# Optimization experiments

Measured on AMD Instinct MI355X. Metric: run time of the kernel, lower is better.

Reference implementation:

```python
import jax, jax.numpy as jnp
import numpy as np

SPARSITY_W = 0.01
SMOOTH_W = 0.1
K = 10  # min(10, N-1) with N >> 10


def setup_inputs() -> dict:
    key = jax.random.key(0)
    k1, k2, k3 = jax.random.split(key, 3)
    N = 16384
    positions = jax.random.normal(k1, (N, 3), dtype=jnp.float32)
    opacities = jax.random.uniform(k2, (N,), dtype=jnp.float32)
    scales = jax.random.uniform(k3, (N, 3), dtype=jnp.float32)
    return {"positions": positions, "opacities": opacities, "scales": scales}


def _pairwise_dist(x):
    # Euclidean cdist(x, x): [N, N]
    sq = jnp.sum(x * x, axis=-1)
    d2 = sq[:, None] + sq[None, :] - 2.0 * (x @ x.T)
    return jnp.sqrt(jnp.maximum(d2, 0.0))


def reference(positions, opacities, scales):
    # sparsity: mean |opacity|
    sparsity_loss = jnp.mean(jnp.abs(opacities))

    # smoothness: kNN (k=10, excluding self) gather + mean |opacity diff|
    dist = _pairwise_dist(positions)                       # [N, N]
    _, idx = jax.lax.top_k(-dist, K + 1)                   # smallest K+1 dists
    nbr_idx = idx[:, 1:]                                   # drop self: [N, K]
    nbr_op = opacities[nbr_idx]                            # [N, K]
    smoothness_loss = jnp.mean(jnp.abs(opacities[:, None] - nbr_op))

    # scale reg: mean |scale - 1|
    scale_loss = jnp.mean(jnp.abs(scales - 1.0))

    # opacity reg: mean (opacity - 0.5)^2
    opacity_loss = jnp.mean((opacities - 0.5) ** 2)

    return (SPARSITY_W * sparsity_loss + SMOOTH_W * smoothness_loss
            + scale_loss + opacity_loss)
```

## Files before the change

kernel.cpp:

```cpp
#include <hip/hip_runtime.h>
#include <stdint.h>

#define NPTS   16384
#define TOPK   10
#define NBX    32
#define NBK    (32 * 32 * 32)
#define XMIN   (-5.0f)
#define INVBW  (3.2f)
#define SENT_STEP 0x4000u
#define NSLOT  256


__device__ __forceinline__ unsigned umin_(unsigned a, unsigned b) { return a < b ? a : b; }
__device__ __forceinline__ unsigned umax_(unsigned a, unsigned b) { return a > b ? a : b; }

__device__ __forceinline__ void chain_insert(unsigned a[TOPK], unsigned key) {
#pragma unroll
    for (int k = TOPK - 1; k > 0; --k) a[k] = umin_(umax_(a[k - 1], key), a[k]);
    a[0] = umin_(a[0], key);
}

__device__ __forceinline__ void ce_(unsigned &x, unsigned &y) {
    unsigned lo = umin_(x, y); y = umax_(x, y); x = lo;
}

__device__ __forceinline__ void bitonic10(unsigned a[TOPK]) {
    ce_(a[0], a[8]); ce_(a[1], a[9]);
    ce_(a[0], a[4]); ce_(a[1], a[5]); ce_(a[2], a[6]); ce_(a[3], a[7]);
    ce_(a[0], a[2]); ce_(a[1], a[3]); ce_(a[4], a[6]); ce_(a[5], a[7]);
    ce_(a[0], a[1]); ce_(a[2], a[3]); ce_(a[4], a[5]); ce_(a[6], a[7]); ce_(a[8], a[9]);
}

__device__ __forceinline__ void merge_shfl(unsigned a[TOPK], int w) {
    unsigned b[TOPK];
#pragma unroll
    for (int k = 0; k < TOPK; ++k) b[k] = (unsigned)__shfl_xor((int)a[k], w, 64);
#pragma unroll
    for (int k = 0; k < TOPK; ++k) a[k] = umin_(a[k], b[TOPK - 1 - k]);
    bitonic10(a);
}

__device__ __forceinline__ void scan2(
    unsigned a[TOPK], const float4* __restrict__ sorted,
    unsigned p0, unsigned p1, unsigned s, float mx, float my, float mz)
{
    float4 c0 = sorted[p0];
    float4 c1 = sorted[p1];
    float dx0 = c0.x - mx, dy0 = c0.y - my, dz0 = c0.z - mz;
    float dx1 = c1.x - mx, dy1 = c1.y - my, dz1 = c1.z - mz;
    float d20 = fmaf(dx0, dx0, fmaf(dy0, dy0, dz0 * dz0));
    float d21 = fmaf(dx1, dx1, fmaf(dy1, dy1, dz1 * dz1));
    unsigned k0 = (__float_as_uint(d20) & 0xFFFFC000u) | p0;
    unsigned k1 = (__float_as_uint(d21) & 0xFFFFC000u) | p1;
    if (p0 == s) k0 = 0xFFFFFFFFu;
    if (p1 == s) k1 = 0xFFFFFFFFu;
    unsigned kmin = umin_(k0, k1), kmax = umax_(k0, k1);
    if (kmin < a[TOPK - 1]) {
        chain_insert(a, kmin);
        if (kmax < a[TOPK - 1]) chain_insert(a, kmax);
    }
}

__device__ __forceinline__ void scan1(
    unsigned a[TOPK], const float4* __restrict__ sorted,
    unsigned p, unsigned s, float mx, float my, float mz)
{
    float4 c = sorted[p];
    float dx = c.x - mx, dy = c.y - my, dz = c.z - mz;
    float d2 = fmaf(dx, dx, fmaf(dy, dy, dz * dz));
    unsigned key = (__float_as_uint(d2) & 0xFFFFC000u) | p;
    if (p == s) key = 0xFFFFFFFFu;
    if (key < a[TOPK - 1]) chain_insert(a, key);
}

__device__ __forceinline__ int cellf(float v) {
    int b = (int)((v - XMIN) * INVBW);
    return min(max(b, 0), NBX - 1);
}

__global__ __launch_bounds__(256) void setup_kernel(
    const float* __restrict__ pos, const float* __restrict__ opac,
    const float* __restrict__ scales, float* __restrict__ parts,
    unsigned* __restrict__ hist)
{
    int i = blockIdx.x * 256 + threadIdx.x;
    float o = opac[i];
    float d = o - 0.5f;
    float s_sp = fabsf(o);
    float s_op = d * d;
    float s_sc = fabsf(scales[3 * i] - 1.0f) + fabsf(scales[3 * i + 1] - 1.0f)
               + fabsf(scales[3 * i + 2] - 1.0f);
    int bx = cellf(pos[3 * i]);
    int by = cellf(pos[3 * i + 1]);
    int bz = cellf(pos[3 * i + 2]);
    atomicAdd(&hist[(bx << 10) | (by << 5) | bz], 1u);
#pragma unroll
    for (int off = 32; off > 0; off >>= 1) {
        s_sp += __shfl_down(s_sp, off, 64);
        s_sc += __shfl_down(s_sc, off, 64);
        s_op += __shfl_down(s_op, off, 64);
    }
    if ((threadIdx.x & 63) == 0) {
        const int row = (blockIdx.x * 4 + (threadIdx.x >> 6)) & (NSLOT - 1);
        atomicAdd(&parts[row * 32 + 0], s_sp);
        atomicAdd(&parts[row * 32 + 1], s_sc);
        atomicAdd(&parts[row * 32 + 2], s_op);
    }
}

__global__ __launch_bounds__(1024) void prefix_scan(
    unsigned* __restrict__ hist, unsigned* __restrict__ base)
{
    __shared__ unsigned wsum[16];
    const int t = threadIdx.x;
    const int lane = t & 63, wid = t >> 6;
    unsigned loc[32];
    uint4* h4 = (uint4*)(hist + t * 32);
#pragma unroll
    for (int j = 0; j < 8; ++j) {
        uint4 h = h4[j];
        loc[4 * j + 0] = h.x; loc[4 * j + 1] = h.y;
        loc[4 * j + 2] = h.z; loc[4 * j + 3] = h.w;
    }
    unsigned run = 0;
#pragma unroll
    for (int j = 0; j < 32; ++j) { unsigned v = loc[j]; loc[j] = run; run += v; }
    unsigned inc = run;
#pragma unroll
    for (int off = 1; off < 64; off <<= 1) {
        unsigned v = (unsigned)__shfl_up((int)inc, off, 64);
        if (lane >= off) inc += v;
    }
    if (lane == 63) wsum[wid] = inc;
    __syncthreads();
    if (wid == 0) {
        unsigned w = (lane < 16) ? wsum[lane] : 0u;
#pragma unroll
        for (int off = 1; off < 16; off <<= 1) {
            unsigned v = (unsigned)__shfl_up((int)w, off, 64);
            if (lane >= off) w += v;
        }
        if (lane < 16) wsum[lane] = w;
    }
    __syncthreads();
    const unsigned wbase = (wid > 0) ? wsum[wid - 1] : 0u;
    const unsigned tbase = wbase + inc - run;
    uint4* b4 = (uint4*)(base + t * 32);
#pragma unroll
    for (int j = 0; j < 8; ++j) {
        b4[j] = make_uint4(loc[4 * j] + tbase, loc[4 * j + 1] + tbase,
                           loc[4 * j + 2] + tbase, loc[4 * j + 3] + tbase);
        h4[j] = make_uint4(0u, 0u, 0u, 0u);
    }
    if (t == 1023) base[NBK] = NPTS;
}

__global__ __launch_bounds__(256) void scatter_sorted(
    const float* __restrict__ pos, const float* __restrict__ opac,
    const unsigned* __restrict__ base, unsigned* __restrict__ cnt,
    float4* __restrict__ sorted)
{
    int i = blockIdx.x * 256 + threadIdx.x;
    float x = pos[3 * i], y = pos[3 * i + 1], z = pos[3 * i + 2];
    int b = (cellf(x) << 10) | (cellf(y) << 5) | cellf(z);
    unsigned p = base[b] + atomicAdd(&cnt[b], 1u);
    sorted[p] = make_float4(x, y, z, opac[i]);
}

__global__ __launch_bounds__(256) void knn_all(
    const float4* __restrict__ sorted, const unsigned* __restrict__ base,
    float* __restrict__ parts)
{
    const int lane = threadIdx.x & 63;
    const int s    = (blockIdx.x * 256 + threadIdx.x) >> 6;

    const float4 me = sorted[s];

    unsigned a[TOPK];
#pragma unroll
    for (int k = 0; k < TOPK; ++k) a[k] = 0xFFFFFFFFu;
    {
        const int dir = lane >> 5;
        const int start = 1 + (lane & 31) * 4;
#pragma unroll
        for (int t = 0; t < 4; ++t) {
            int p = dir ? (s - start - t) : (s + start + t);
            int pc = min(max(p, 0), NPTS - 1);
            float4 c = sorted[pc];
            float dx = c.x - me.x, dy = c.y - me.y, dz = c.z - me.z;
            float d2 = fmaf(dx, dx, fmaf(dy, dy, dz * dz));
            unsigned key = (__float_as_uint(d2) & 0xFFFFC000u) | (unsigned)pc;
            if (p < 0 || p >= NPTS) key = 0xFFFFFFFFu;
            chain_insert(a, key);
        }
    }
    merge_shfl(a, 1);  merge_shfl(a, 2);  merge_shfl(a, 4);
    merge_shfl(a, 8);  merge_shfl(a, 16); merge_shfl(a, 32);
    const unsigned sentinel = (a[TOPK - 1] & 0xFFFFC000u) + SENT_STEP;
    const float R = sqrtf(__uint_as_float(sentinel)) + 1e-6f;

    const int bxlo = cellf(me.x - R), bxhi = cellf(me.x + R);
    const int bylo = cellf(me.y - R), byhi = cellf(me.y + R);
    const int bzlo = cellf(me.z - R), bzhi = cellf(me.z + R);
    const int nyw   = byhi - bylo + 1;
    const int npair = (bxhi - bxlo + 1) * nyw;

#pragma unroll
    for (int k = 0; k < TOPK; ++k) a[k] = sentinel;

    const int grp = lane >> 3;
    const int gl  = lane & 7;

    for (int cbase = 0; cbase < npair; cbase += 64) {
        const int cnum = min(64, npair - cbase);
        unsigned mylo = 0, myhi = 0;
        const int pi = cbase + lane;
        if (pi < npair) {
            const int qx = pi / nyw;
            const int cb = ((bxlo + qx) << 10) | ((bylo + pi - qx * nyw) << 5);
            mylo = base[cb + bzlo];
            myhi = base[cb + bzhi + 1];
        }
        for (int j = grp; j < cnum; j += 8) {
            const unsigned lo = (unsigned)__shfl((int)mylo, j, 64);
            const unsigned hi = (unsigned)__shfl((int)myhi, j, 64);
            unsigned p = lo + gl;
            for (; p + 8 < hi; p += 16)
                scan2(a, sorted, p, p + 8, (unsigned)s, me.x, me.y, me.z);
            if (p < hi)
                scan1(a, sorted, p, (unsigned)s, me.x, me.y, me.z);
        }
    }

    merge_shfl(a, 1);  merge_shfl(a, 2);  merge_shfl(a, 4);
    merge_shfl(a, 8);  merge_shfl(a, 16); merge_shfl(a, 32);

    float v = 0.0f;
    if (lane < TOPK) {
        int j = (int)(a[lane] & 0x3FFFu);
        v = fabsf(me.w - sorted[j].w);
    }
    v += __shfl_down(v, 8, 64);
    v += __shfl_down(v, 4, 64);
    v += __shfl_down(v, 2, 64);
    v += __shfl_down(v, 1, 64);
    if (lane == 0)
        atomicAdd(&parts[(s & (NSLOT - 1)) * 32 + 3], v);
}

__global__ void combine(const float* __restrict__ parts, float* __restrict__ out)
{
    const int lane = threadIdx.x;
    float sp = 0.0f, sc = 0.0f, op = 0.0f, sm = 0.0f;
#pragma unroll
    for (int r = 0; r < NSLOT / 64; ++r) {
        float4 p = *(const float4*)(parts + (r * 64 + lane) * 32);
        sp += p.x; sc += p.y; op += p.z; sm += p.w;
    }
#pragma unroll
    for (int off = 32; off > 0; off >>= 1) {
        sp += __shfl_down(sp, off, 64);
        sc += __shfl_down(sc, off, 64);
        op += __shfl_down(op, off, 64);
        sm += __shfl_down(sm, off, 64);
    }
    if (lane == 0) {
        const float n = (float)NPTS;
        out[0] = 0.01f * (sp / n) + 0.1f * (sm / (n * 10.0f))
               + sc / (3.0f * n) + op / n;
    }
}

extern "C" void kernel_launch(void* const* d_in, const int* in_sizes, int n_in,
                              void* d_out, int out_size, void* d_ws, size_t ws_size,
                              hipStream_t stream)
{
    const float* pos    = (const float*)d_in[0];
    const float* opac   = (const float*)d_in[1];
    const float* scales = (const float*)d_in[2];
    float* out = (float*)d_out;

    char* ws = (char*)d_ws;
    float*    parts  = (float*)(ws + 128);
    unsigned* histcnt= (unsigned*)(ws + 33024);
    unsigned* base   = (unsigned*)(ws + 164096);
    float4*   sorted = (float4*)(ws + 295296);

    hipMemsetAsync(ws, 0, 164096, stream);

    setup_kernel  <<<NPTS / 256, 256, 0, stream>>>(pos, opac, scales, parts, histcnt);
    prefix_scan   <<<1, 1024, 0, stream>>>(histcnt, base);
    scatter_sorted<<<NPTS / 256, 256, 0, stream>>>(pos, opac, base, histcnt, sorted);
    knn_all       <<<NPTS / 4, 256, 0, stream>>>(sorted, base, parts);
    combine       <<<1, 64, 0, stream>>>(parts, out);
}
```

Before: 112.8 us.

## Fuse histogram, scan and scatter into one cooperative kernel; sort initial kNN keys

Merges the setup, single-block prefix scan and scatter kernels into one cooperative kernel with grid-wide syncs. The atomic rank from the histogram pass is reused for the scatter, so the second atomic pass is gone, and the scan is spread over 64 blocks. This removes two launch gaps and the serial single-block scan, at the cost of three grid.sync barriers. It also replaces four chain inserts in the kNN seeding with a 4-element sorting network before the shuffle merges.

```diff
diff --git a/kernel.cpp b/kernel.cpp
--- a/kernel.cpp
+++ b/kernel.cpp
@@ -1,5 +1,8 @@
 #include <hip/hip_runtime.h>
+#include <hip/hip_cooperative_groups.h>
 #include <stdint.h>
+
+namespace cg = cooperative_groups;
 
 #define NPTS   16384
 #define TOPK   10
@@ -9,6 +12,7 @@
 #define INVBW  (3.2f)
 #define SENT_STEP 0x4000u
 #define NSLOT  256
+#define PRE_BLOCKS 64
 
 
 __device__ __forceinline__ unsigned umin_(unsigned a, unsigned b) { return a < b ? a : b; }
@@ -78,93 +82,77 @@
     return min(max(b, 0), NBX - 1);
 }
 
-__global__ __launch_bounds__(256) void setup_kernel(
+__global__ __launch_bounds__(256) void preprocess(
     const float* __restrict__ pos, const float* __restrict__ opac,
     const float* __restrict__ scales, float* __restrict__ parts,
-    unsigned* __restrict__ hist)
-{
-    int i = blockIdx.x * 256 + threadIdx.x;
-    float o = opac[i];
+    unsigned* __restrict__ hist, unsigned* __restrict__ blocksum,
+    unsigned* __restrict__ base, float4* __restrict__ sorted)
+{
+    cg::grid_group grid = cg::this_grid();
+    const int tid  = blockIdx.x * 256 + threadIdx.x;
+    const int lane = threadIdx.x & 63;
+    const int wv   = threadIdx.x >> 6;
+
+    const float x = pos[3 * tid], y = pos[3 * tid + 1], z = pos[3 * tid + 2];
+    const float o = opac[tid];
     float d = o - 0.5f;
     float s_sp = fabsf(o);
     float s_op = d * d;
-    float s_sc = fabsf(scales[3 * i] - 1.0f) + fabsf(scales[3 * i + 1] - 1.0f)
-               + fabsf(scales[3 * i + 2] - 1.0f);
-    int bx = cellf(pos[3 * i]);
-    int by = cellf(pos[3 * i + 1]);
-    int bz = cellf(pos[3 * i + 2]);
-    atomicAdd(&hist[(bx << 10) | (by << 5) | bz], 1u);
+    float s_sc = fabsf(scales[3 * tid] - 1.0f) + fabsf(scales[3 * tid + 1] - 1.0f)
+               + fabsf(scales[3 * tid + 2] - 1.0f);
+    const int b = (cellf(x) << 10) | (cellf(y) << 5) | cellf(z);
+    const unsigned rank = atomicAdd(&hist[b], 1u);
 #pragma unroll
     for (int off = 32; off > 0; off >>= 1) {
         s_sp += __shfl_down(s_sp, off, 64);
         s_sc += __shfl_down(s_sc, off, 64);
         s_op += __shfl_down(s_op, off, 64);
     }
-    if ((threadIdx.x & 63) == 0) {
-        const int row = (blockIdx.x * 4 + (threadIdx.x >> 6)) & (NSLOT - 1);
+    if (lane == 0) {
+        const int row = (blockIdx.x * 4 + wv) & (NSLOT - 1);
         atomicAdd(&parts[row * 32 + 0], s_sp);
         atomicAdd(&parts[row * 32 + 1], s_sc);
         atomicAdd(&parts[row * 32 + 2], s_op);
     }
-}
-
-__global__ __launch_bounds__(1024) void prefix_scan(
-    unsigned* __restrict__ hist, unsigned* __restrict__ base)
-{
-    __shared__ unsigned wsum[16];
-    const int t = threadIdx.x;
-    const int lane = t & 63, wid = t >> 6;
-    unsigned loc[32];
-    uint4* h4 = (uint4*)(hist + t * 32);
-#pragma unroll
-    for (int j = 0; j < 8; ++j) {
-        uint4 h = h4[j];
-        loc[4 * j + 0] = h.x; loc[4 * j + 1] = h.y;
-        loc[4 * j + 2] = h.z; loc[4 * j + 3] = h.w;
-    }
-    unsigned run = 0;
-#pragma unroll
-    for (int j = 0; j < 32; ++j) { unsigned v = loc[j]; loc[j] = run; run += v; }
-    unsigned inc = run;
+
+    grid.sync();
+
+    const unsigned h0 = hist[2 * tid], h1 = hist[2 * tid + 1];
+    const unsigned tot = h0 + h1;
+    unsigned inc = tot;
 #pragma unroll
     for (int off = 1; off < 64; off <<= 1) {
         unsigned v = (unsigned)__shfl_up((int)inc, off, 64);
         if (lane >= off) inc += v;
     }
-    if (lane == 63) wsum[wid] = inc;
+    __shared__ unsigned lws[4];
+    __shared__ unsigned s_bpref;
+    if (lane == 63) lws[wv] = inc;
     __syncthreads();
-    if (wid == 0) {
-        unsigned w = (lane < 16) ? wsum[lane] : 0u;
-#pragma unroll
-        for (int off = 1; off < 16; off <<= 1) {
-            unsigned v = (unsigned)__shfl_up((int)w, off, 64);
-            if (lane >= off) w += v;
-        }
-        if (lane < 16) wsum[lane] = w;
+    unsigned woff = 0;
+    for (int w = 0; w < wv; ++w) woff += lws[w];
+    if (threadIdx.x == 0)
+        blocksum[blockIdx.x] = lws[0] + lws[1] + lws[2] + lws[3];
+
+    grid.sync();
+
+    if (wv == 0) {
+        unsigned bsv = blocksum[lane];
+        unsigned mine = ((unsigned)lane < blockIdx.x) ? bsv : 0u;
+#pragma unroll
+        for (int off = 32; off > 0; off >>= 1)
+            mine += (unsigned)__shfl_xor((int)mine, off, 64);
+        if (lane == 0) s_bpref = mine;
     }
     __syncthreads();
-    const unsigned wbase = (wid > 0) ? wsum[wid - 1] : 0u;
-    const unsigned tbase = wbase + inc - run;
-    uint4* b4 = (uint4*)(base + t * 32);
-#pragma unroll
-    for (int j = 0; j < 8; ++j) {
-        b4[j] = make_uint4(loc[4 * j] + tbase, loc[4 * j + 1] + tbase,
-                           loc[4 * j + 2] + tbase, loc[4 * j + 3] + tbase);
-        h4[j] = make_uint4(0u, 0u, 0u, 0u);
-    }
-    if (t == 1023) base[NBK] = NPTS;
-}
-
-__global__ __launch_bounds__(256) void scatter_sorted(
-    const float* __restrict__ pos, const float* __restrict__ opac,
-    const unsigned* __restrict__ base, unsigned* __restrict__ cnt,
-    float4* __restrict__ sorted)
-{
-    int i = blockIdx.x * 256 + threadIdx.x;
-    float x = pos[3 * i], y = pos[3 * i + 1], z = pos[3 * i + 2];
-    int b = (cellf(x) << 10) | (cellf(y) << 5) | cellf(z);
-    unsigned p = base[b] + atomicAdd(&cnt[b], 1u);
-    sorted[p] = make_float4(x, y, z, opac[i]);
+    const unsigned tb = s_bpref + woff + (inc - tot);
+    base[2 * tid]     = tb;
+    base[2 * tid + 1] = tb + h0;
+    if (tid == NPTS - 1) base[NBK] = (unsigned)NPTS;
+
+    grid.sync();
+
+    sorted[base[b] + rank] = make_float4(x, y, z, o);
 }
 
 __global__ __launch_bounds__(256) void knn_all(
@@ -176,9 +164,7 @@
 
     const float4 me = sorted[s];
 
-    unsigned a[TOPK];
-#pragma unroll
-    for (int k = 0; k < TOPK; ++k) a[k] = 0xFFFFFFFFu;
+    unsigned kk[4];
     {
         const int dir = lane >> 5;
         const int start = 1 + (lane & 31) * 4;
@@ -191,9 +177,15 @@
             float d2 = fmaf(dx, dx, fmaf(dy, dy, dz * dz));
             unsigned key = (__float_as_uint(d2) & 0xFFFFC000u) | (unsigned)pc;
             if (p < 0 || p >= NPTS) key = 0xFFFFFFFFu;
-            chain_insert(a, key);
+            kk[t] = key;
         }
     }
+    ce_(kk[0], kk[2]); ce_(kk[1], kk[3]); ce_(kk[0], kk[1]);
+    ce_(kk[2], kk[3]); ce_(kk[1], kk[2]);
+    unsigned a[TOPK];
+    a[0] = kk[0]; a[1] = kk[1]; a[2] = kk[2]; a[3] = kk[3];
+#pragma unroll
+    for (int k = 4; k < TOPK; ++k) a[k] = 0xFFFFFFFFu;
     merge_shfl(a, 1);  merge_shfl(a, 2);  merge_shfl(a, 4);
     merge_shfl(a, 8);  merge_shfl(a, 16); merge_shfl(a, 32);
     const unsigned sentinel = (a[TOPK - 1] & 0xFFFFC000u) + SENT_STEP;
@@ -281,16 +273,19 @@
     float* out = (float*)d_out;
 
     char* ws = (char*)d_ws;
-    float*    parts  = (float*)(ws + 128);
-    unsigned* histcnt= (unsigned*)(ws + 33024);
-    unsigned* base   = (unsigned*)(ws + 164096);
-    float4*   sorted = (float4*)(ws + 295296);
+    float*    parts    = (float*)(ws + 128);
+    unsigned* hist     = (unsigned*)(ws + 33024);
+    unsigned* blocksum = (unsigned*)(ws + 164096);
+    unsigned* base     = (unsigned*)(ws + 164352);
+    float4*   sorted   = (float4*)(ws + 295552);
 
     hipMemsetAsync(ws, 0, 164096, stream);
 
-    setup_kernel  <<<NPTS / 256, 256, 0, stream>>>(pos, opac, scales, parts, histcnt);
-    prefix_scan   <<<1, 1024, 0, stream>>>(histcnt, base);
-    scatter_sorted<<<NPTS / 256, 256, 0, stream>>>(pos, opac, base, histcnt, sorted);
-    knn_all       <<<NPTS / 4, 256, 0, stream>>>(sorted, base, parts);
-    combine       <<<1, 64, 0, stream>>>(parts, out);
-}
+    void* args[] = { (void*)&pos, (void*)&opac, (void*)&scales, (void*)&parts,
+                     (void*)&hist, (void*)&blocksum, (void*)&base, (void*)&sorted };
+    hipLaunchCooperativeKernel(preprocess, dim3(PRE_BLOCKS), dim3(256),
+                               args, 0, stream);
+
+    knn_all<<<NPTS / 4, 256, 0, stream>>>(sorted, base, parts);
+    combine<<<1, 64, 0, stream>>>(parts, out);
+}
```

Measured after the change: 146.7 us. 30.1% more time.
